# Kernel tuning notes

Measured on AMD Instinct MI355X. Metric: run time of the kernel, lower is better.

Reference implementation:

```python
import jax, jax.numpy as jnp
import numpy as np

PAD = 0  # padding_index
BIG = 10000.0

B, S = 1024, 128
V, E, H, T = 200, 512, 512, 24


def setup_inputs() -> dict:
    key = jax.random.key(0)
    ks = jax.random.split(key, 12)
    sequences = jax.random.randint(ks[0], (B, S), 0, V, dtype=jnp.int32)
    labels = jax.random.randint(ks[1], (B, S), 0, T, dtype=jnp.int32)
    true_lengths = jax.random.randint(ks[2], (B,), 1, S, dtype=jnp.int32)
    emb = jax.random.normal(ks[3], (V, E), dtype=jnp.float32) * 0.1
    emb = emb.at[PAD].set(0.0)  # nn.Embedding padding_idx zeros that row
    w1 = jax.random.normal(ks[4], (H, H), dtype=jnp.float32) * (1.0 / np.sqrt(H))
    b1 = jax.random.normal(ks[5], (H,), dtype=jnp.float32) * 0.01
    w2 = jax.random.normal(ks[6], (T, H), dtype=jnp.float32) * (1.0 / np.sqrt(H))
    b2 = jax.random.normal(ks[7], (T,), dtype=jnp.float32) * 0.01
    start_trans = jax.random.uniform(ks[8], (T,), jnp.float32, -0.1, 0.1)
    end_trans = jax.random.uniform(ks[9], (T,), jnp.float32, -0.1, 0.1)
    transitions = jax.random.uniform(ks[10], (T, T), jnp.float32, -0.1, 0.1)
    return {"sequences": sequences, "labels": labels, "true_lengths": true_lengths,
            "emb": emb, "w1": w1, "b1": b1, "w2": w2, "b2": b2,
            "start_trans": start_trans, "end_trans": end_trans, "transitions": transitions}


def _emissions(sequences, emb, w1, b1, w2, b2):
    pad_mask = (sequences == PAD).astype(jnp.float32)  # [B,S]
    x = emb[sequences]                                  # [B,S,E]
    h = jax.nn.relu(x @ w1.T + b1)                      # [B,S,H]
    scores = jax.nn.relu(h @ w2.T + b2)                 # [B,S,T]
    scores = scores.at[:, :, PAD].add(pad_mask * BIG)
    return scores


def _crf_nll_mean(emissions, labels, start_trans, end_trans, transitions):
    # emissions [B,S,T], labels [B,S]; mask = all ones (none passed in forward)
    # numerator: score of gold path
    em_gold = jnp.take_along_axis(emissions, labels[..., None], axis=2)[..., 0]  # [B,S]
    num = (start_trans[labels[:, 0]]
           + em_gold.sum(axis=1)
           + transitions[labels[:, :-1], labels[:, 1:]].sum(axis=1)
           + end_trans[labels[:, -1]])  # [B]
    # denominator: forward algorithm via scan over time
    em_t = jnp.swapaxes(emissions, 0, 1)  # [S,B,T]
    alpha0 = start_trans[None, :] + em_t[0]  # [B,T]

    def step(alpha, emit):
        # alpha [B,T_prev], transitions [T_prev,T_next], emit [B,T_next]
        nxt = jax.nn.logsumexp(alpha[:, :, None] + transitions[None] + emit[:, None, :], axis=1)
        return nxt, None

    alpha, _ = jax.lax.scan(step, alpha0, em_t[1:])
    denom = jax.nn.logsumexp(alpha + end_trans[None, :], axis=1)  # [B]
    llh = num - denom
    return -jnp.mean(llh)


def reference(sequences, labels, true_lengths, emb, w1, b1, w2, b2,
              start_trans, end_trans, transitions):
    emissions = _emissions(sequences, emb, w1, b1, w2, b2)
    return _crf_nll_mean(emissions, labels, start_trans, end_trans, transitions)
```

## Files before the change

### kernel.cpp

```cpp
#include <hip/hip_runtime.h>
#include <math.h>

#define PAD_IDX 0
#define BIGV 10000.0f
constexpr int B_ = 1024, S_ = 128, V_ = 200, E_ = 512, H_ = 512, T_ = 24;

constexpr int OFF_H  = 262144;
constexpr int OFF_EM = 364544;
constexpr int OFF_W  = 369344;
constexpr int OFF_MX = 374144;

__global__ __launch_bounds__(256) void transpose_kernel(
    const float* __restrict__ w1, float* __restrict__ w1T,
    float* __restrict__ out)
{
    __shared__ float tile[64][65];
    const int bi = blockIdx.x >> 3, bj = blockIdx.x & 7;
    const int tx = threadIdx.x & 63, r0 = (threadIdx.x >> 6) * 16;
    if (blockIdx.x == 0 && threadIdx.x == 0) out[0] = 0.f;
    #pragma unroll
    for (int m = 0; m < 16; ++m) {
        const int r = r0 + m;
        tile[r][tx] = w1[(size_t)(bi * 64 + r) * 512 + bj * 64 + tx];
    }
    __syncthreads();
    #pragma unroll
    for (int m = 0; m < 16; ++m) {
        const int r = r0 + m;
        w1T[(size_t)(bj * 64 + r) * 512 + bi * 64 + tx] = tile[tx][r];
    }
}

__global__ __launch_bounds__(256) void h_kernel(
    const float* __restrict__ emb, const float* __restrict__ w1T,
    const float* __restrict__ b1, float* __restrict__ h_ws)
{
    __shared__ float xi[2 * E_];
    __shared__ float part_s[4][64][8];
    const int pair = blockIdx.x >> 1, half = blockIdx.x & 1;
    const int v0 = pair * 2, v1 = v0 + 1;
    const int tid = threadIdx.x;

    {
        const float* __restrict__ x0 = emb + (size_t)v0 * E_;
        const float* __restrict__ x1 = emb + (size_t)v1 * E_;
        #pragma unroll
        for (int m = 0; m < 2; ++m) {
            const int k = tid + m * 256;
            xi[2 * k]     = x0[k];
            xi[2 * k + 1] = x1[k];
        }
    }
    __syncthreads();

    const int part = tid >> 6;
    const int quad = tid & 63;
    const int t0 = half * 256 + quad * 4;
    const int k0 = part * 128;

    float a0 = 0.f, a1 = 0.f, a2 = 0.f, a3 = 0.f;
    float c0 = 0.f, c1 = 0.f, c2 = 0.f, c3 = 0.f;
    const float4* __restrict__ wp = (const float4*)(w1T + (size_t)k0 * H_ + t0);
    const float2* __restrict__ xp = (const float2*)xi + k0;
    #pragma unroll 4
    for (int i = 0; i < 128; ++i) {
        const float4 w = wp[(size_t)i * (H_ / 4)];
        const float2 x = xp[i];
        a0 = fmaf(w.x, x.x, a0); a1 = fmaf(w.y, x.x, a1);
        a2 = fmaf(w.z, x.x, a2); a3 = fmaf(w.w, x.x, a3);
        c0 = fmaf(w.x, x.y, c0); c1 = fmaf(w.y, x.y, c1);
        c2 = fmaf(w.z, x.y, c2); c3 = fmaf(w.w, x.y, c3);
    }
    part_s[part][quad][0] = a0; part_s[part][quad][1] = a1;
    part_s[part][quad][2] = a2; part_s[part][quad][3] = a3;
    part_s[part][quad][4] = c0; part_s[part][quad][5] = c1;
    part_s[part][quad][6] = c2; part_s[part][quad][7] = c3;
    __syncthreads();

    {
        const int q2 = tid >> 2, r0 = tid & 3;
        const float s0 = (part_s[0][q2][r0]     + part_s[1][q2][r0])
                       + (part_s[2][q2][r0]     + part_s[3][q2][r0]);
        const float s1 = (part_s[0][q2][r0 + 4] + part_s[1][q2][r0 + 4])
                       + (part_s[2][q2][r0 + 4] + part_s[3][q2][r0 + 4]);
        const int t = half * 256 + tid;
        const float bb = b1[t];
        h_ws[(size_t)v0 * H_ + t] = fmaxf(s0 + bb, 0.f);
        h_ws[(size_t)v1 * H_ + t] = fmaxf(s1 + bb, 0.f);
    }
}

__global__ __launch_bounds__(256) void emis_kernel(
    const float* __restrict__ h_ws, const float* __restrict__ w2,
    const float* __restrict__ b2, float* __restrict__ em_table,
    float* __restrict__ w_table, float* __restrict__ emax_arr)
{
    __shared__ float em_row[32];
    const int v = blockIdx.x;
    const int t = threadIdx.x;
    const int wave = t >> 6, lane = t & 63;
    const float* __restrict__ hrow = h_ws + (size_t)v * H_;

    for (int jj2 = 0; jj2 < 6; ++jj2) {
        const int jo = wave * 6 + jj2;
        float part = 0.f;
        #pragma unroll
        for (int m = 0; m < H_ / 64; ++m) {
            const int k = lane + m * 64;
            part = fmaf(hrow[k], w2[(size_t)jo * H_ + k], part);
        }
        #pragma unroll
        for (int off = 32; off; off >>= 1)
            part += __shfl_xor(part, off, 64);
        if (lane == 0) {
            float val = fmaxf(part + b2[jo], 0.f);
            if (v == 0 && jo == PAD_IDX) val += BIGV;
            em_row[jo] = val;
        }
    }
    __syncthreads();

    if (t < 32) {
        float x = (t < T_) ? em_row[t] : -INFINITY;
        float mx = x;
        #pragma unroll
        for (int off = 16; off; off >>= 1)
            mx = fmaxf(mx, __shfl_xor(mx, off, 32));
        if (t < T_) {
            em_table[v * T_ + t] = x;
            w_table[v * T_ + t]  = __expf(x - mx);
        }
        if (t == 0) emax_arr[v] = mx;
    }
}

#define ACC4(base)                                                              \
    s0 = fmaf(__uint_as_float(__builtin_amdgcn_ds_swizzle(qi, (base) << 5)),     \
              Ecol[(base)], s0);                                                \
    s1 = fmaf(__uint_as_float(__builtin_amdgcn_ds_swizzle(qi, ((base)+1) << 5)), \
              Ecol[(base)+1], s1);                                              \
    s2 = fmaf(__uint_as_float(__builtin_amdgcn_ds_swizzle(qi, ((base)+2) << 5)), \
              Ecol[(base)+2], s2);                                              \
    s3 = fmaf(__uint_as_float(__builtin_amdgcn_ds_swizzle(qi, ((base)+3) << 5)), \
              Ecol[(base)+3], s3);

__global__ __launch_bounds__(128) void crf_kernel(
    const int* __restrict__ seq, const int* __restrict__ labels,
    const float* __restrict__ start_t, const float* __restrict__ end_t,
    const float* __restrict__ trans, const float* __restrict__ em_table,
    const float* __restrict__ w_table, const float* __restrict__ emax_arr,
    float* __restrict__ out)
{
    __shared__ __align__(16) float w_s[V_ * T_];
    __shared__ float emax_s[V_];
    __shared__ int   tok_s[4 * S_];
    const int tid = threadIdx.x;
    {
        const float4* __restrict__ src = (const float4*)w_table;
        float4* dst = (float4*)w_s;
        for (int i = tid; i < V_ * T_ / 4; i += 128) dst[i] = src[i];
    }
    for (int i = tid; i < V_; i += 128) emax_s[i] = emax_arr[i];
    {
        const int base = blockIdx.x * 4 * S_;
        #pragma unroll
        for (int i = 0; i < 4; ++i)
            tok_s[tid + i * 128] = seq[base + tid + i * 128];
    }
    __syncthreads();

    const int grp = tid >> 5, j = tid & 31;
    const int b = blockIdx.x * 4 + grp;
    const int jj = (j < T_) ? j : 0;
    const bool act = (j < T_);
    const int* __restrict__ lrow = labels + (size_t)b * S_;
    const int* __restrict__ tks  = tok_s + grp * S_;

    float Ecol[T_];
    #pragma unroll
    for (int i = 0; i < T_; ++i)
        Ecol[i] = __expf(trans[i * T_ + jj]);

    const int tok0 = tks[0];
    const float a0 = start_t[jj] + em_table[tok0 * T_ + jj];
    float m0 = a0;
    #pragma unroll
    for (int off = 16; off; off >>= 1)
        m0 = fmaxf(m0, __shfl_xor(m0, off, 32));
    float q = __expf(a0 - m0);
    float logacc = m0;

    float wv; int tokB;
    { const int tA = tks[1]; wv = w_s[tA * T_ + jj]; tokB = tks[2]; }

    for (int s = 1; s < S_; ++s) {
        const float wn = w_s[tokB * T_ + jj];
        const int tokC = tks[(s + 2 < S_) ? s + 2 : S_ - 1];
        const unsigned qi = __float_as_uint(q);
        float s0 = 0.f, s1 = 0.f, s2 = 0.f, s3 = 0.f;
        ACC4(0) ACC4(4) ACC4(8) ACC4(12) ACC4(16) ACC4(20)
        q = ((s0 + s1) + (s2 + s3)) * wv;
        wv = wn; tokB = tokC;
        if ((s & 15) == 0) {
            float m = q;
            #pragma unroll
            for (int off = 16; off; off >>= 1)
                m = fmaxf(m, __shfl_xor(m, off, 32));
            q *= (1.0f / m);
            logacc += __logf(m);
        }
    }

    float fin = act ? q * __expf(end_t[jj]) : 0.f;
    #pragma unroll
    for (int off = 16; off; off >>= 1)
        fin += __shfl_xor(fin, off, 32);
    const float denom_part = logacc + __logf(fin);

    float gp = 0.f;
    #pragma unroll
    for (int r = 0; r < 4; ++r) {
        const int s = j + r * 32;
        const int tk = tks[s];
        const int ls = lrow[s];
        gp += em_table[tk * T_ + ls];
        if (s >= 1) gp -= emax_s[tk];
        if (s < S_ - 1) gp += trans[ls * T_ + lrow[s + 1]];
        if (s == 0) gp += start_t[ls];
        if (s == S_ - 1) gp += end_t[ls];
    }
    #pragma unroll
    for (int off = 16; off; off >>= 1)
        gp += __shfl_xor(gp, off, 32);

    if (j == 0)
        atomicAdd(out, (denom_part - gp) * (1.0f / (float)B_));
}

extern "C" void kernel_launch(void* const* d_in, const int* in_sizes, int n_in,
                              void* d_out, int out_size, void* d_ws, size_t ws_size,
                              hipStream_t stream) {
    const int*   seq     = (const int*)d_in[0];
    const int*   labels  = (const int*)d_in[1];
    const float* emb     = (const float*)d_in[3];
    const float* w1      = (const float*)d_in[4];
    const float* b1      = (const float*)d_in[5];
    const float* w2      = (const float*)d_in[6];
    const float* b2      = (const float*)d_in[7];
    const float* start_t = (const float*)d_in[8];
    const float* end_t   = (const float*)d_in[9];
    const float* trans   = (const float*)d_in[10];

    float* ws       = (float*)d_ws;
    float* w1T      = ws;
    float* h_ws     = ws + OFF_H;
    float* em_table = ws + OFF_EM;
    float* w_table  = ws + OFF_W;
    float* emax_arr = ws + OFF_MX;
    float* out      = (float*)d_out;

    transpose_kernel<<<64, 256, 0, stream>>>(w1, w1T, out);
    h_kernel<<<200, 256, 0, stream>>>(emb, w1T, b1, h_ws);
    emis_kernel<<<V_, 256, 0, stream>>>(h_ws, w2, b2, em_table, w_table, emax_arr);
    crf_kernel<<<B_ / 4, 128, 0, stream>>>(seq, labels, start_t, end_t, trans,
                                           em_table, w_table, emax_arr, out);
}
```

Measured before the change: 120.0 us.

## Interleave two CRF sequences per half-wave and store transposed W1 in bf16

The CRF kernel now has each 32-lane group run the forward recursion for two batch rows at once. Interleaving the two independent dependency chains is meant to hide ds_swizzle and FMA latency in the serial scan. It halves the threads per block while keeping four sequences per block. Separately, the transposed W1 is written as bf16 and unpacked in h_kernel to halve its weight read traffic, at the cost of reduced precision in the hidden-layer matmul.

```diff
diff --git a/kernel.cpp b/kernel.cpp
--- a/kernel.cpp
+++ b/kernel.cpp
@@ -10,8 +10,14 @@
 constexpr int OFF_W  = 369344;
 constexpr int OFF_MX = 374144;
 
+__device__ __forceinline__ unsigned short f2bf(float f) {
+    unsigned u = __float_as_uint(f);
+    u += 0x7fffu + ((u >> 16) & 1u);
+    return (unsigned short)(u >> 16);
+}
+
 __global__ __launch_bounds__(256) void transpose_kernel(
-    const float* __restrict__ w1, float* __restrict__ w1T,
+    const float* __restrict__ w1, unsigned short* __restrict__ w1Tb,
     float* __restrict__ out)
 {
     __shared__ float tile[64][65];
@@ -27,12 +33,12 @@
     #pragma unroll
     for (int m = 0; m < 16; ++m) {
         const int r = r0 + m;
-        w1T[(size_t)(bj * 64 + r) * 512 + bi * 64 + tx] = tile[tx][r];
+        w1Tb[(size_t)(bj * 64 + r) * 512 + bi * 64 + tx] = f2bf(tile[tx][r]);
     }
 }
 
 __global__ __launch_bounds__(256) void h_kernel(
-    const float* __restrict__ emb, const float* __restrict__ w1T,
+    const float* __restrict__ emb, const unsigned short* __restrict__ w1Tb,
     const float* __restrict__ b1, float* __restrict__ h_ws)
 {
     __shared__ float xi[2 * E_];
@@ -60,16 +66,20 @@
 
     float a0 = 0.f, a1 = 0.f, a2 = 0.f, a3 = 0.f;
     float c0 = 0.f, c1 = 0.f, c2 = 0.f, c3 = 0.f;
-    const float4* __restrict__ wp = (const float4*)(w1T + (size_t)k0 * H_ + t0);
+    const unsigned short* __restrict__ wp = w1Tb + (size_t)k0 * H_ + t0;
     const float2* __restrict__ xp = (const float2*)xi + k0;
     #pragma unroll 4
     for (int i = 0; i < 128; ++i) {
-        const float4 w = wp[(size_t)i * (H_ / 4)];
+        const uint2 wu = *(const uint2*)(wp + (size_t)i * H_);
         const float2 x = xp[i];
-        a0 = fmaf(w.x, x.x, a0); a1 = fmaf(w.y, x.x, a1);
-        a2 = fmaf(w.z, x.x, a2); a3 = fmaf(w.w, x.x, a3);
-        c0 = fmaf(w.x, x.y, c0); c1 = fmaf(w.y, x.y, c1);
-        c2 = fmaf(w.z, x.y, c2); c3 = fmaf(w.w, x.y, c3);
+        const float w0 = __uint_as_float(wu.x << 16);
+        const float w1v = __uint_as_float(wu.x & 0xffff0000u);
+        const float w2v = __uint_as_float(wu.y << 16);
+        const float w3v = __uint_as_float(wu.y & 0xffff0000u);
+        a0 = fmaf(w0,  x.x, a0); a1 = fmaf(w1v, x.x, a1);
+        a2 = fmaf(w2v, x.x, a2); a3 = fmaf(w3v, x.x, a3);
+        c0 = fmaf(w0,  x.y, c0); c1 = fmaf(w1v, x.y, c1);
+        c2 = fmaf(w2v, x.y, c2); c3 = fmaf(w3v, x.y, c3);
     }
     part_s[part][quad][0] = a0; part_s[part][quad][1] = a1;
     part_s[part][quad][2] = a2; part_s[part][quad][3] = a3;
@@ -134,17 +144,18 @@
     }
 }
 
-#define ACC4(base)                                                              \
-    s0 = fmaf(__uint_as_float(__builtin_amdgcn_ds_swizzle(qi, (base) << 5)),     \
-              Ecol[(base)], s0);                                                \
-    s1 = fmaf(__uint_as_float(__builtin_amdgcn_ds_swizzle(qi, ((base)+1) << 5)), \
-              Ecol[(base)+1], s1);                                              \
-    s2 = fmaf(__uint_as_float(__builtin_amdgcn_ds_swizzle(qi, ((base)+2) << 5)), \
-              Ecol[(base)+2], s2);                                              \
-    s3 = fmaf(__uint_as_float(__builtin_amdgcn_ds_swizzle(qi, ((base)+3) << 5)), \
-              Ecol[(base)+3], s3);
-
-__global__ __launch_bounds__(128) void crf_kernel(
+#define BC(q, i) __uint_as_float(__builtin_amdgcn_ds_swizzle((q), (i) << 5))
+#define ACC4D(base)                                                   \
+    sA0 = fmaf(BC(qiA, (base)),     Ecol[(base)],     sA0);           \
+    sB0 = fmaf(BC(qiB, (base)),     Ecol[(base)],     sB0);           \
+    sA1 = fmaf(BC(qiA, (base) + 1), Ecol[(base) + 1], sA1);           \
+    sB1 = fmaf(BC(qiB, (base) + 1), Ecol[(base) + 1], sB1);           \
+    sA2 = fmaf(BC(qiA, (base) + 2), Ecol[(base) + 2], sA2);           \
+    sB2 = fmaf(BC(qiB, (base) + 2), Ecol[(base) + 2], sB2);           \
+    sA3 = fmaf(BC(qiA, (base) + 3), Ecol[(base) + 3], sA3);           \
+    sB3 = fmaf(BC(qiB, (base) + 3), Ecol[(base) + 3], sB3);
+
+__global__ __launch_bounds__(64) void crf_kernel(
     const int* __restrict__ seq, const int* __restrict__ labels,
     const float* __restrict__ start_t, const float* __restrict__ end_t,
     const float* __restrict__ trans, const float* __restrict__ em_table,
@@ -158,83 +169,116 @@
     {
         const float4* __restrict__ src = (const float4*)w_table;
         float4* dst = (float4*)w_s;
-        for (int i = tid; i < V_ * T_ / 4; i += 128) dst[i] = src[i];
-    }
-    for (int i = tid; i < V_; i += 128) emax_s[i] = emax_arr[i];
+        for (int i = tid; i < V_ * T_ / 4; i += 64) dst[i] = src[i];
+    }
+    for (int i = tid; i < V_; i += 64) emax_s[i] = emax_arr[i];
     {
         const int base = blockIdx.x * 4 * S_;
         #pragma unroll
-        for (int i = 0; i < 4; ++i)
-            tok_s[tid + i * 128] = seq[base + tid + i * 128];
+        for (int i = 0; i < 8; ++i)
+            tok_s[tid + i * 64] = seq[base + tid + i * 64];
     }
     __syncthreads();
 
     const int grp = tid >> 5, j = tid & 31;
-    const int b = blockIdx.x * 4 + grp;
+    const int bA = blockIdx.x * 4 + grp * 2;
     const int jj = (j < T_) ? j : 0;
     const bool act = (j < T_);
-    const int* __restrict__ lrow = labels + (size_t)b * S_;
-    const int* __restrict__ tks  = tok_s + grp * S_;
+    const int* __restrict__ lrowA = labels + (size_t)bA * S_;
+    const int* __restrict__ lrowB = lrowA + S_;
+    const int* __restrict__ tksA  = tok_s + grp * 2 * S_;
+    const int* __restrict__ tksB  = tksA + S_;
 
     float Ecol[T_];
     #pragma unroll
     for (int i = 0; i < T_; ++i)
         Ecol[i] = __expf(trans[i * T_ + jj]);
 
-    const int tok0 = tks[0];
-    const float a0 = start_t[jj] + em_table[tok0 * T_ + jj];
-    float m0 = a0;
-    #pragma unroll
-    for (int off = 16; off; off >>= 1)
-        m0 = fmaxf(m0, __shfl_xor(m0, off, 32));
-    float q = __expf(a0 - m0);
-    float logacc = m0;
-
-    float wv; int tokB;
-    { const int tA = tks[1]; wv = w_s[tA * T_ + jj]; tokB = tks[2]; }
+    const float st = start_t[jj];
+    float qA, qB, logaccA, logaccB;
+    {
+        const float aA = st + em_table[tksA[0] * T_ + jj];
+        const float aB = st + em_table[tksB[0] * T_ + jj];
+        float mA = aA, mB = aB;
+        #pragma unroll
+        for (int off = 16; off; off >>= 1) {
+            mA = fmaxf(mA, __shfl_xor(mA, off, 32));
+            mB = fmaxf(mB, __shfl_xor(mB, off, 32));
+        }
+        qA = __expf(aA - mA); qB = __expf(aB - mB);
+        logaccA = mA; logaccB = mB;
+    }
+
+    float wvA, wvB; int tokA, tokB;
+    wvA = w_s[tksA[1] * T_ + jj]; tokA = tksA[2];
+    wvB = w_s[tksB[1] * T_ + jj]; tokB = tksB[2];
 
     for (int s = 1; s < S_; ++s) {
-        const float wn = w_s[tokB * T_ + jj];
-        const int tokC = tks[(s + 2 < S_) ? s + 2 : S_ - 1];
-        const unsigned qi = __float_as_uint(q);
-        float s0 = 0.f, s1 = 0.f, s2 = 0.f, s3 = 0.f;
-        ACC4(0) ACC4(4) ACC4(8) ACC4(12) ACC4(16) ACC4(20)
-        q = ((s0 + s1) + (s2 + s3)) * wv;
-        wv = wn; tokB = tokC;
+        const float wnA = w_s[tokA * T_ + jj];
+        const float wnB = w_s[tokB * T_ + jj];
+        const int nxt = (s + 2 < S_) ? s + 2 : S_ - 1;
+        const int tokA2 = tksA[nxt], tokB2 = tksB[nxt];
+        const unsigned qiA = __float_as_uint(qA);
+        const unsigned qiB = __float_as_uint(qB);
+        float sA0 = 0.f, sA1 = 0.f, sA2 = 0.f, sA3 = 0.f;
+        float sB0 = 0.f, sB1 = 0.f, sB2 = 0.f, sB3 = 0.f;
+        ACC4D(0) ACC4D(4) ACC4D(8) ACC4D(12) ACC4D(16) ACC4D(20)
+        qA = ((sA0 + sA1) + (sA2 + sA3)) * wvA;
+        qB = ((sB0 + sB1) + (sB2 + sB3)) * wvB;
+        wvA = wnA; tokA = tokA2;
+        wvB = wnB; tokB = tokB2;
         if ((s & 15) == 0) {
-            float m = q;
+            float mA = qA, mB = qB;
             #pragma unroll
-            for (int off = 16; off; off >>= 1)
-                m = fmaxf(m, __shfl_xor(m, off, 32));
-            q *= (1.0f / m);
-            logacc += __logf(m);
-        }
-    }
-
-    float fin = act ? q * __expf(end_t[jj]) : 0.f;
-    #pragma unroll
-    for (int off = 16; off; off >>= 1)
-        fin += __shfl_xor(fin, off, 32);
-    const float denom_part = logacc + __logf(fin);
-
-    float gp = 0.f;
+            for (int off = 16; off; off >>= 1) {
+                mA = fmaxf(mA, __shfl_xor(mA, off, 32));
+                mB = fmaxf(mB, __shfl_xor(mB, off, 32));
+            }
+            qA *= (1.0f / mA); qB *= (1.0f / mB);
+            logaccA += __logf(mA); logaccB += __logf(mB);
+        }
+    }
+
+    const float ee = __expf(end_t[jj]);
+    float finA = act ? qA * ee : 0.f;
+    float finB = act ? qB * ee : 0.f;
+    #pragma unroll
+    for (int off = 16; off; off >>= 1) {
+        finA += __shfl_xor(finA, off, 32);
+        finB += __shfl_xor(finB, off, 32);
+    }
+    const float denA = logaccA + __logf(finA);
+    const float denB = logaccB + __logf(finB);
+
+    float gpA = 0.f, gpB = 0.f;
     #pragma unroll
     for (int r = 0; r < 4; ++r) {
         const int s = j + r * 32;
-        const int tk = tks[s];
-        const int ls = lrow[s];
-        gp += em_table[tk * T_ + ls];
-        if (s >= 1) gp -= emax_s[tk];
-        if (s < S_ - 1) gp += trans[ls * T_ + lrow[s + 1]];
-        if (s == 0) gp += start_t[ls];
-        if (s == S_ - 1) gp += end_t[ls];
-    }
-    #pragma unroll
-    for (int off = 16; off; off >>= 1)
-        gp += __shfl_xor(gp, off, 32);
+        {
+            const int tk = tksA[s], ls = lrowA[s];
+            gpA += em_table[tk * T_ + ls];
+            if (s >= 1) gpA -= emax_s[tk];
+            if (s < S_ - 1) gpA += trans[ls * T_ + lrowA[s + 1]];
+            if (s == 0) gpA += start_t[ls];
+            if (s == S_ - 1) gpA += end_t[ls];
+        }
+        {
+            const int tk = tksB[s], ls = lrowB[s];
+            gpB += em_table[tk * T_ + ls];
+            if (s >= 1) gpB -= emax_s[tk];
+            if (s < S_ - 1) gpB += trans[ls * T_ + lrowB[s + 1]];
+            if (s == 0) gpB += start_t[ls];
+            if (s == S_ - 1) gpB += end_t[ls];
+        }
+    }
+    #pragma unroll
+    for (int off = 16; off; off >>= 1) {
+        gpA += __shfl_xor(gpA, off, 32);
+        gpB += __shfl_xor(gpB, off, 32);
+    }
 
     if (j == 0)
-        atomicAdd(out, (denom_part - gp) * (1.0f / (float)B_));
+        atomicAdd(out, ((denA - gpA) + (denB - gpB)) * (1.0f / (float)B_));
 }
 
 extern "C" void kernel_launch(void* const* d_in, const int* in_sizes, int n_in,
@@ -252,16 +296,16 @@
     const float* trans   = (const float*)d_in[10];
 
     float* ws       = (float*)d_ws;
-    float* w1T      = ws;
+    unsigned short* w1Tb = (unsigned short*)d_ws;
     float* h_ws     = ws + OFF_H;
     float* em_table = ws + OFF_EM;
     float* w_table  = ws + OFF_W;
     float* emax_arr = ws + OFF_MX;
     float* out      = (float*)d_out;
 
-    transpose_kernel<<<64, 256, 0, stream>>>(w1, w1T, out);
-    h_kernel<<<200, 256, 0, stream>>>(emb, w1T, b1, h_ws);
+    transpose_kernel<<<64, 256, 0, stream>>>(w1, w1Tb, out);
+    h_kernel<<<200, 256, 0, stream>>>(emb, w1Tb, b1, h_ws);
     emis_kernel<<<V_, 256, 0, stream>>>(h_ws, w2, b2, em_table, w_table, emax_arr);
-    crf_kernel<<<B_ / 4, 128, 0, stream>>>(seq, labels, start_t, end_t, trans,
-                                           em_table, w_table, emax_arr, out);
-}
+    crf_kernel<<<B_ / 4, 64, 0, stream>>>(seq, labels, start_t, end_t, trans,
+                                          em_table, w_table, emax_arr, out);
+}
```

New measurement: 133.8 us. +11.4%, slower.

## Split CRF partition recursion into forward and backward halves; store w1T as bf16

Applied to the files above, without the earlier changes.

Each sequence now uses a 64-lane wave. The first 32 lanes run the forward recursion over the first half of the sequence, and the other 32 run a backward recursion from the end. The two halves are joined with one extra transition step and a dot product, which halves the serial dependency chain of the scaled-probability recursion. Separately, the transposed w1 is stored as bf16 to halve the weight bytes read in the hidden-layer kernel, at the cost of reduced precision in the emissions.

```diff
diff --git a/kernel.cpp b/kernel.cpp
--- a/kernel.cpp
+++ b/kernel.cpp
@@ -10,8 +10,14 @@
 constexpr int OFF_W  = 369344;
 constexpr int OFF_MX = 374144;
 
+__device__ __forceinline__ unsigned short f2bf(float f) {
+    unsigned u = __float_as_uint(f);
+    u += 0x7fffu + ((u >> 16) & 1u);
+    return (unsigned short)(u >> 16);
+}
+
 __global__ __launch_bounds__(256) void transpose_kernel(
-    const float* __restrict__ w1, float* __restrict__ w1T,
+    const float* __restrict__ w1, unsigned short* __restrict__ w1Tb,
     float* __restrict__ out)
 {
     __shared__ float tile[64][65];
@@ -27,12 +33,12 @@
     #pragma unroll
     for (int m = 0; m < 16; ++m) {
         const int r = r0 + m;
-        w1T[(size_t)(bj * 64 + r) * 512 + bi * 64 + tx] = tile[tx][r];
+        w1Tb[(size_t)(bj * 64 + r) * 512 + bi * 64 + tx] = f2bf(tile[tx][r]);
     }
 }
 
 __global__ __launch_bounds__(256) void h_kernel(
-    const float* __restrict__ emb, const float* __restrict__ w1T,
+    const float* __restrict__ emb, const unsigned short* __restrict__ w1Tb,
     const float* __restrict__ b1, float* __restrict__ h_ws)
 {
     __shared__ float xi[2 * E_];
@@ -60,16 +66,20 @@
 
     float a0 = 0.f, a1 = 0.f, a2 = 0.f, a3 = 0.f;
     float c0 = 0.f, c1 = 0.f, c2 = 0.f, c3 = 0.f;
-    const float4* __restrict__ wp = (const float4*)(w1T + (size_t)k0 * H_ + t0);
+    const unsigned short* __restrict__ wp = w1Tb + (size_t)k0 * H_ + t0;
     const float2* __restrict__ xp = (const float2*)xi + k0;
     #pragma unroll 4
     for (int i = 0; i < 128; ++i) {
-        const float4 w = wp[(size_t)i * (H_ / 4)];
+        const uint2 wu = *(const uint2*)(wp + (size_t)i * H_);
         const float2 x = xp[i];
-        a0 = fmaf(w.x, x.x, a0); a1 = fmaf(w.y, x.x, a1);
-        a2 = fmaf(w.z, x.x, a2); a3 = fmaf(w.w, x.x, a3);
-        c0 = fmaf(w.x, x.y, c0); c1 = fmaf(w.y, x.y, c1);
-        c2 = fmaf(w.z, x.y, c2); c3 = fmaf(w.w, x.y, c3);
+        const float w0 = __uint_as_float(wu.x << 16);
+        const float w1v = __uint_as_float(wu.x & 0xffff0000u);
+        const float w2v = __uint_as_float(wu.y << 16);
+        const float w3v = __uint_as_float(wu.y & 0xffff0000u);
+        a0 = fmaf(w0,  x.x, a0); a1 = fmaf(w1v, x.x, a1);
+        a2 = fmaf(w2v, x.x, a2); a3 = fmaf(w3v, x.x, a3);
+        c0 = fmaf(w0,  x.y, c0); c1 = fmaf(w1v, x.y, c1);
+        c2 = fmaf(w2v, x.y, c2); c3 = fmaf(w3v, x.y, c3);
     }
     part_s[part][quad][0] = a0; part_s[part][quad][1] = a1;
     part_s[part][quad][2] = a2; part_s[part][quad][3] = a3;
@@ -134,17 +144,14 @@
     }
 }
 
-#define ACC4(base)                                                              \
-    s0 = fmaf(__uint_as_float(__builtin_amdgcn_ds_swizzle(qi, (base) << 5)),     \
-              Ecol[(base)], s0);                                                \
-    s1 = fmaf(__uint_as_float(__builtin_amdgcn_ds_swizzle(qi, ((base)+1) << 5)), \
-              Ecol[(base)+1], s1);                                              \
-    s2 = fmaf(__uint_as_float(__builtin_amdgcn_ds_swizzle(qi, ((base)+2) << 5)), \
-              Ecol[(base)+2], s2);                                              \
-    s3 = fmaf(__uint_as_float(__builtin_amdgcn_ds_swizzle(qi, ((base)+3) << 5)), \
-              Ecol[(base)+3], s3);
-
-__global__ __launch_bounds__(128) void crf_kernel(
+#define BC(q, i) __uint_as_float(__builtin_amdgcn_ds_swizzle((q), (i) << 5))
+#define ACC4U(base)                                      \
+    s0 = fmaf(BC(qi, (base)),     Ecoef[(base)],     s0); \
+    s1 = fmaf(BC(qi, (base) + 1), Ecoef[(base) + 1], s1); \
+    s2 = fmaf(BC(qi, (base) + 2), Ecoef[(base) + 2], s2); \
+    s3 = fmaf(BC(qi, (base) + 3), Ecoef[(base) + 3], s3);
+
+__global__ __launch_bounds__(256) void crf_kernel(
     const int* __restrict__ seq, const int* __restrict__ labels,
     const float* __restrict__ start_t, const float* __restrict__ end_t,
     const float* __restrict__ trans, const float* __restrict__ em_table,
@@ -158,49 +165,60 @@
     {
         const float4* __restrict__ src = (const float4*)w_table;
         float4* dst = (float4*)w_s;
-        for (int i = tid; i < V_ * T_ / 4; i += 128) dst[i] = src[i];
-    }
-    for (int i = tid; i < V_; i += 128) emax_s[i] = emax_arr[i];
+        for (int i = tid; i < V_ * T_ / 4; i += 256) dst[i] = src[i];
+    }
+    for (int i = tid; i < V_; i += 256) emax_s[i] = emax_arr[i];
     {
         const int base = blockIdx.x * 4 * S_;
         #pragma unroll
-        for (int i = 0; i < 4; ++i)
-            tok_s[tid + i * 128] = seq[base + tid + i * 128];
-    }
-    __syncthreads();
-
-    const int grp = tid >> 5, j = tid & 31;
-    const int b = blockIdx.x * 4 + grp;
-    const int jj = (j < T_) ? j : 0;
-    const bool act = (j < T_);
+        for (int i = 0; i < 2; ++i)
+            tok_s[tid + i * 256] = seq[base + tid + i * 256];
+    }
+    __syncthreads();
+
+    const int wave = tid >> 6, lane = tid & 63;
+    const int b = blockIdx.x * 4 + wave;
+    const int jl = lane & 31;
+    const int jj = (jl < T_) ? jl : 0;
+    const bool act = (jl < T_);
+    const bool isF = (lane < 32);
     const int* __restrict__ lrow = labels + (size_t)b * S_;
-    const int* __restrict__ tks  = tok_s + grp * S_;
-
-    float Ecol[T_];
-    #pragma unroll
-    for (int i = 0; i < T_; ++i)
-        Ecol[i] = __expf(trans[i * T_ + jj]);
-
-    const int tok0 = tks[0];
-    const float a0 = start_t[jj] + em_table[tok0 * T_ + jj];
-    float m0 = a0;
+    const int* __restrict__ tks  = tok_s + wave * S_;
+
+    float Ecoef[T_];
+    #pragma unroll
+    for (int i = 0; i < T_; ++i) {
+        const int tix = isF ? (i * T_ + jj) : (jj * T_ + i);
+        Ecoef[i] = act ? __expf(trans[tix]) : 0.f;
+    }
+
+    const int tokI = isF ? tks[0] : tks[S_ - 1];
+    const float bse = isF ? start_t[jj] : end_t[jj];
+    const float a0v = bse + em_table[tokI * T_ + jj];
+    float m0 = act ? a0v : -INFINITY;
     #pragma unroll
     for (int off = 16; off; off >>= 1)
         m0 = fmaxf(m0, __shfl_xor(m0, off, 32));
-    float q = __expf(a0 - m0);
-    float logacc = m0;
-
-    float wv; int tokB;
-    { const int tA = tks[1]; wv = w_s[tA * T_ + jj]; tokB = tks[2]; }
-
-    for (int s = 1; s < S_; ++s) {
-        const float wn = w_s[tokB * T_ + jj];
-        const int tokC = tks[(s + 2 < S_) ? s + 2 : S_ - 1];
+    const float qFi = __expf(a0v - m0);
+    const float qBi = w_s[tokI * T_ + jj] * __expf(bse);
+    float q = act ? (isF ? qFi : qBi) : 0.f;
+    float logacc = isF ? m0 : 0.f;
+
+    const int dir_l = isF ? 1 : -1;
+    const int off_l = isF ? 0 : 127;
+
+    float wv = w_s[tks[off_l + dir_l] * T_ + jj];
+    int tokN = tks[off_l + dir_l * 2];
+
+    for (int s = 1; s <= 63; ++s) {
+        const float wn = w_s[tokN * T_ + jj];
+        const int nxt = (s + 2 <= 63) ? s + 2 : 63;
+        const int tokC = tks[off_l + dir_l * nxt];
         const unsigned qi = __float_as_uint(q);
         float s0 = 0.f, s1 = 0.f, s2 = 0.f, s3 = 0.f;
-        ACC4(0) ACC4(4) ACC4(8) ACC4(12) ACC4(16) ACC4(20)
+        ACC4U(0) ACC4U(4) ACC4U(8) ACC4U(12) ACC4U(16) ACC4U(20)
         q = ((s0 + s1) + (s2 + s3)) * wv;
-        wv = wn; tokB = tokC;
+        wv = wn; tokN = tokC;
         if ((s & 15) == 0) {
             float m = q;
             #pragma unroll
@@ -211,16 +229,36 @@
         }
     }
 
-    float fin = act ? q * __expf(end_t[jj]) : 0.f;
-    #pragma unroll
-    for (int off = 16; off; off >>= 1)
-        fin += __shfl_xor(fin, off, 32);
-    const float denom_part = logacc + __logf(fin);
+    {
+        float m = q;
+        #pragma unroll
+        for (int off = 16; off; off >>= 1)
+            m = fmaxf(m, __shfl_xor(m, off, 32));
+        q *= (1.0f / m);
+        logacc += __logf(m);
+    }
+
+    float u;
+    {
+        const unsigned qi = __float_as_uint(q);
+        float s0 = 0.f, s1 = 0.f, s2 = 0.f, s3 = 0.f;
+        ACC4U(0) ACC4U(4) ACC4U(8) ACC4U(12) ACC4U(16) ACC4U(20)
+        u = (s0 + s1) + (s2 + s3);
+    }
+
+    const float sel = isF ? u : q;
+    const float oth = __shfl_xor(sel, 32, 64);
+    float prod = sel * oth;
+    #pragma unroll
+    for (int off = 32; off; off >>= 1)
+        prod += __shfl_xor(prod, off, 64);
+    const float logacc_o = __shfl_xor(logacc, 32, 64);
+    const float denom = logacc + logacc_o + __logf(0.5f * prod);
 
     float gp = 0.f;
     #pragma unroll
-    for (int r = 0; r < 4; ++r) {
-        const int s = j + r * 32;
+    for (int r = 0; r < 2; ++r) {
+        const int s = lane + r * 64;
         const int tk = tks[s];
         const int ls = lrow[s];
         gp += em_table[tk * T_ + ls];
@@ -230,11 +268,11 @@
         if (s == S_ - 1) gp += end_t[ls];
     }
     #pragma unroll
-    for (int off = 16; off; off >>= 1)
-        gp += __shfl_xor(gp, off, 32);
-
-    if (j == 0)
-        atomicAdd(out, (denom_part - gp) * (1.0f / (float)B_));
+    for (int off = 32; off; off >>= 1)
+        gp += __shfl_xor(gp, off, 64);
+
+    if (lane == 0)
+        atomicAdd(out, (denom - gp) * (1.0f / (float)B_));
 }
 
 extern "C" void kernel_launch(void* const* d_in, const int* in_sizes, int n_in,
@@ -252,16 +290,16 @@
     const float* trans   = (const float*)d_in[10];
 
     float* ws       = (float*)d_ws;
-    float* w1T      = ws;
+    unsigned short* w1Tb = (unsigned short*)d_ws;
     float* h_ws     = ws + OFF_H;
     float* em_table = ws + OFF_EM;
     float* w_table  = ws + OFF_W;
     float* emax_arr = ws + OFF_MX;
     float* out      = (float*)d_out;
 
-    transpose_kernel<<<64, 256, 0, stream>>>(w1, w1T, out);
-    h_kernel<<<200, 256, 0, stream>>>(emb, w1T, b1, h_ws);
+    transpose_kernel<<<64, 256, 0, stream>>>(w1, w1Tb, out);
+    h_kernel<<<200, 256, 0, stream>>>(emb, w1Tb, b1, h_ws);
     emis_kernel<<<V_, 256, 0, stream>>>(h_ws, w2, b2, em_table, w_table, emax_arr);
-    crf_kernel<<<B_ / 4, 128, 0, stream>>>(seq, labels, start_t, end_t, trans,
+    crf_kernel<<<B_ / 4, 256, 0, stream>>>(seq, labels, start_t, end_t, trans,
                                            em_table, w_table, emax_arr, out);
 }
```

New measurement: 121.2 us. About the same (+1.0%).
